# Optimization experiments

Hardware: AMD Instinct MI355X
Metric: run time of the kernel (lower is better)

Reference implementation:

```python
import jax, jax.numpy as jnp
import numpy as np

B = 16384          # tokens
H = 2048           # hidden_size
E = 8              # num_experts
K = 2              # top-k
HF = H // 4        # expert bottleneck dim


def setup_inputs() -> dict:
    key = jax.random.key(0)
    k0, k1, k2, k3 = jax.random.split(key, 4)
    scale = lambda kk, shape, fan: jax.random.normal(kk, shape, jnp.float32) * (1.0 / np.sqrt(fan))
    x = jax.random.normal(k0, (B, H), jnp.float32)
    W1 = scale(k1, (E, H, HF), H)      # experts[e][0].weight (transposed)
    b1 = jnp.zeros((E, HF), jnp.float32)
    W2 = scale(k2, (E, HF), HF)        # experts[e][2].weight (out dim 1, no bias)
    Wg = scale(k3, (H, E), H)          # gate.weight (transposed)
    bg = jnp.zeros((E,), jnp.float32)
    return {"x": x, "W1": W1, "b1": b1, "W2": W2, "Wg": Wg, "bg": bg}


def reference(x, W1, b1, W2, Wg, bg):
    # Gating (eval mode: no noise branch)
    logits = x @ Wg + bg                                  # [B, E]
    top_w, top_i = jax.lax.top_k(logits, K)               # [B, K]
    w = jax.nn.softmax(top_w, axis=-1)                    # [B, K]
    # Scatter top-k softmax weights into dense combine weights [B, E];
    # unselected experts get weight 0, so the dense all-expert compute
    # below is mathematically identical to the masked dispatch loop.
    combine = jnp.zeros_like(logits).at[jnp.arange(x.shape[0])[:, None], top_i].add(w)
    # All-expert MLP: Linear -> exact GELU -> Linear(->1, no bias)
    h = jax.nn.gelu(jnp.einsum('bh,ehf->bef', x, W1) + b1, approximate=False)  # [B, E, HF]
    o = jnp.einsum('bef,ef->be', h, W2)                   # [B, E]
    final_scores = jnp.sum(combine * o, axis=-1, keepdims=True)  # [B, 1]
    return final_scores, logits
```

## Files before the change

kernel.cpp:

```cpp
#include <hip/hip_runtime.h>
#include <math.h>

#define B_TOK 16384
#define H_DIM 2048
#define NE    8
#define TOPK  2
#define HFD   512

#define BK 32
#define NKSTEP (H_DIM / BK)
#define PTMAX 129
#define PROWS 33792

static constexpr size_t OFF_COUNTS = 0;
static constexpr size_t OFF_CBASE  = 128;
static constexpr size_t OFF_BUCKET = 1024;
static constexpr size_t OFF_WSLOT  = 525312;
static constexpr size_t OFF_ROUTE  = 656384;
static constexpr size_t OFF_INV    = 721920;
static constexpr size_t OFF_WGT    = 1u << 20;
static constexpr size_t OFF_P2     = 1572864;
static constexpr size_t OFF_W1H    = 4u << 20;
static constexpr size_t OFF_XGT    = 20971520;

typedef short bfrag __attribute__((ext_vector_type(8)));
typedef float facc  __attribute__((ext_vector_type(16)));

__device__ inline unsigned short f2bf(float f) {
    union { float f; unsigned u; } v; v.f = f;
    unsigned r = v.u + 0x7FFFu + ((v.u >> 16) & 1u);
    return (unsigned short)(r >> 16);
}
__device__ inline unsigned pack2(float lo, float hi) {
    return (unsigned)f2bf(lo) | ((unsigned)f2bf(hi) << 16);
}

__global__ __launch_bounds__(256)
void wg_transpose_kernel(const float* __restrict__ Wg,
                         float* __restrict__ WgT)
{
    const int t = threadIdx.x;
    #pragma unroll
    for (int rep = 0; rep < H_DIM / 256; ++rep) {
        const int h = rep * 256 + t;
        const float4 a = *reinterpret_cast<const float4*>(Wg + (size_t)h * NE);
        const float4 b = *reinterpret_cast<const float4*>(Wg + (size_t)h * NE + 4);
        #pragma unroll
        for (int rr = 0; rr < 8; ++rr) {
            float* W = WgT + (size_t)rr * (NE * H_DIM);
            W[0 * H_DIM + h] = a.x;  W[1 * H_DIM + h] = a.y;
            W[2 * H_DIM + h] = a.z;  W[3 * H_DIM + h] = a.w;
            W[4 * H_DIM + h] = b.x;  W[5 * H_DIM + h] = b.y;
            W[6 * H_DIM + h] = b.z;  W[7 * H_DIM + h] = b.w;
        }
    }
}

__global__ __launch_bounds__(256)
void prep_w1_kernel(const float* __restrict__ W1,
                    unsigned short* __restrict__ W1h)
{
    const int e     = blockIdx.x >> 6;
    const int kstep = blockIdx.x & 63;
    const int tid   = threadIdx.x;

    const float* src = W1 + ((size_t)e * H_DIM + kstep * BK) * HFD;

    #pragma unroll
    for (int s = 0; s < 4; ++s) {
        #pragma unroll
        for (int fh = 0; fh < 2; ++fh) {
            const int f = fh * 256 + tid;
            float v[8];
            #pragma unroll
            for (int j = 0; j < 8; ++j)
                v[j] = src[(size_t)(s * 8 + j) * HFD + f];
            uint4 p;
            p.x = pack2(v[0], v[1]); p.y = pack2(v[2], v[3]);
            p.z = pack2(v[4], v[5]); p.w = pack2(v[6], v[7]);
            *reinterpret_cast<uint4*>(
                W1h + ((size_t)((e * 2 + fh) * 64 + kstep)) * 8192
                    + (s * 256 + tid) * 8) = p;
        }
    }
}

__global__ __launch_bounds__(256)
void gate_logits_kernel(const float* __restrict__ x,
                        const float* __restrict__ WgT,
                        const float* __restrict__ bg,
                        float* __restrict__ out_logits,
                        float* __restrict__ wslot,
                        int*   __restrict__ route)
{
    __shared__ float Wlds[NE * H_DIM];

    const int tid = threadIdx.x;
    const float* Wsrc = WgT + (size_t)(blockIdx.x & 7) * (NE * H_DIM);
    #pragma unroll
    for (int i = 0; i < (NE * H_DIM) / (256 * 4); ++i) {
        const int idx = (i * 256 + tid) * 4;
        *reinterpret_cast<float4*>(&Wlds[idx]) =
            *reinterpret_cast<const float4*>(Wsrc + idx);
    }
    __syncthreads();

    const int w = tid >> 6, l = tid & 63;
    const int tbase = blockIdx.x * 64 + w * 16;

    for (int pass = 0; pass < 4; ++pass) {
        const int t0 = tbase + pass * 4;
        float acc[4][NE];
        #pragma unroll
        for (int j = 0; j < 4; ++j)
            #pragma unroll
            for (int e = 0; e < NE; ++e) acc[j][e] = 0.f;

        for (int i = 0; i < 8; ++i) {
            const int h = i * 256 + 4 * l;
            float4 xv[4];
            #pragma unroll
            for (int j = 0; j < 4; ++j)
                xv[j] = *reinterpret_cast<const float4*>(
                    x + (size_t)(t0 + j) * H_DIM + h);
            #pragma unroll
            for (int e = 0; e < NE; ++e) {
                const float4 wv = *reinterpret_cast<const float4*>(&Wlds[e * H_DIM + h]);
                #pragma unroll
                for (int j = 0; j < 4; ++j)
                    acc[j][e] += xv[j].x * wv.x + xv[j].y * wv.y
                               + xv[j].z * wv.z + xv[j].w * wv.w;
            }
        }

        #pragma unroll
        for (int j = 0; j < 4; ++j)
            #pragma unroll
            for (int e = 0; e < NE; ++e)
                #pragma unroll
                for (int off = 32; off > 0; off >>= 1)
                    acc[j][e] += __shfl_xor(acc[j][e], off, 64);

        if (l == 0) {
            #pragma unroll
            for (int j = 0; j < 4; ++j) {
                const int tok = t0 + j;
                float lg[NE];
                #pragma unroll
                for (int e = 0; e < NE; ++e) lg[e] = acc[j][e] + bg[e];

                float4* lo = reinterpret_cast<float4*>(out_logits + (size_t)tok * NE);
                lo[0] = make_float4(lg[0], lg[1], lg[2], lg[3]);
                lo[1] = make_float4(lg[4], lg[5], lg[6], lg[7]);

                int i0 = 0; float v0 = lg[0];
                #pragma unroll
                for (int e = 1; e < NE; ++e)
                    if (lg[e] > v0) { v0 = lg[e]; i0 = e; }
                int i1 = -1; float v1 = -3.4e38f;
                #pragma unroll
                for (int e = 0; e < NE; ++e)
                    if (e != i0 && lg[e] > v1) { v1 = lg[e]; i1 = e; }

                const float w0 = 1.f / (1.f + expf(v1 - v0));
                wslot[tok * 2]     = w0;
                wslot[tok * 2 + 1] = 1.f - w0;
                route[tok] = i0 | (i1 << 8);
            }
        }
    }
}

__global__ __launch_bounds__(1024)
void route_kernel(const int* __restrict__ route,
                  int* __restrict__ counts,
                  int* __restrict__ bucket)
{
    __shared__ int lcnt[NE];
    __shared__ int lbase[NE];
    const int tid = threadIdx.x;
    const int tok = blockIdx.x * 1024 + tid;

    if (tid < NE) lcnt[tid] = 0;
    __syncthreads();

    const int rt = route[tok];
    const int i0 = rt & 255;
    const int i1 = rt >> 8;
    const int r0 = atomicAdd(&lcnt[i0], 1);
    const int r1 = atomicAdd(&lcnt[i1], 1);
    __syncthreads();

    if (tid < NE) lbase[tid] = atomicAdd(&counts[tid], lcnt[tid]);
    __syncthreads();

    bucket[i0 * B_TOK + lbase[i0] + r0] = tok * 2;
    bucket[i1 * B_TOK + lbase[i1] + r1] = tok * 2 + 1;
}

__global__ void prefix_kernel(const int* __restrict__ counts,
                              int* __restrict__ cbase)
{
    if (threadIdx.x == 0 && blockIdx.x == 0) {
        int acc = 0;
        for (int e = 0; e < NE; ++e) {
            const int cp = ((counts[e] + 127) >> 7) << 7;
            cbase[e]      = acc;
            cbase[NE + e] = cp;
            acc += cp;
        }
    }
}

__global__ __launch_bounds__(256)
void xgather_kernel(const float* __restrict__ x,
                    const int* __restrict__ bucket,
                    const int* __restrict__ counts,
                    const int* __restrict__ cbase,
                    unsigned short* __restrict__ xgT,
                    int* __restrict__ inv)
{
    const int e    = blockIdx.x & 7;
    const int tile = blockIdx.x >> 3;
    const int n    = counts[e];
    const int pos0 = tile * 64;
    if (pos0 >= n) return;
    const int cb   = cbase[e];
    const size_t cpad = (size_t)cbase[NE + e];
    const int t = threadIdx.x;

    __shared__ int toks[64];
    __shared__ unsigned short T[8][64][8];

    if (t < 64) {
        const int pos = pos0 + t;
        const int entry = bucket[e * B_TOK + min(pos, n - 1)];
        toks[t] = entry >> 1;
        if (pos < n) inv[entry] = cb + pos;
    }
    __syncthreads();

    const int p = t >> 2;
    const int q = t & 3;
    const float* src = x + (size_t)toks[p] * H_DIM + q * 16;
    unsigned short* dstbase = xgT + (size_t)cb * H_DIM;

    for (int kc = 0; kc < 32; ++kc) {
        const float4 v0 = *reinterpret_cast<const float4*>(src + kc * 64);
        const float4 v1 = *reinterpret_cast<const float4*>(src + kc * 64 + 4);
        const float4 v2 = *reinterpret_cast<const float4*>(src + kc * 64 + 8);
        const float4 v3 = *reinterpret_cast<const float4*>(src + kc * 64 + 12);
        uint4 pa, pb;
        pa.x = pack2(v0.x, v0.y); pa.y = pack2(v0.z, v0.w);
        pa.z = pack2(v1.x, v1.y); pa.w = pack2(v1.z, v1.w);
        pb.x = pack2(v2.x, v2.y); pb.y = pack2(v2.z, v2.w);
        pb.z = pack2(v3.x, v3.y); pb.w = pack2(v3.z, v3.w);
        __syncthreads();
        *reinterpret_cast<uint4*>(&T[q * 2][p][0])     = pa;
        *reinterpret_cast<uint4*>(&T[q * 2 + 1][p][0]) = pb;
        __syncthreads();
        #pragma unroll
        for (int g = 0; g < 2; ++g) {
            const int u   = t + g * 256;
            const int s8  = u >> 6;
            const int pp  = u & 63;
            const int kst = 2 * kc + (s8 >> 2);
            const int sl  = s8 & 3;
            *reinterpret_cast<uint4*>(
                dstbase + ((size_t)(kst * 4 + sl) * cpad + pos0 + pp) * 8) =
                *reinterpret_cast<const uint4*>(&T[s8][pp][0]);
        }
    }
}

__global__ __launch_bounds__(256, 2)
void expert_mfma_kernel(const unsigned short* __restrict__ xgT,
                        const unsigned short* __restrict__ W1h,
                        const float* __restrict__ b1,
                        const float* __restrict__ W2,
                        const int* __restrict__ counts,
                        const int* __restrict__ cbase,
                        float* __restrict__ P2)
{
    const int e  = blockIdx.x & 7;
    const int r  = blockIdx.x >> 3;
    const int fh = r & 1;
    const int pt = r >> 1;
    const int n  = counts[e];
    const int pos0 = pt * 128;
    if (pos0 >= n) return;
    const int nt = min(128, n - pos0);
    const int cb = cbase[e];
    const size_t cpad = (size_t)cbase[NE + e];

    __shared__ float o_part[2][128];

    const int tid = threadIdx.x;
    const int w   = tid >> 6;
    const int l   = tid & 63;
    const int lo5 = l & 31;
    const int hi  = l >> 5;
    const int wm  = w & 1;
    const int wf  = w >> 1;

    const unsigned short* Wimg = W1h + (size_t)((e * 2 + fh) * 64) * 8192;
    const unsigned short* xg_e = xgT + (size_t)cb * H_DIM;

    const size_t posm0 = (size_t)pos0 + wm * 64 + lo5;
    const size_t posm1 = posm0 + 32;

    facc acc[2][4];
    #pragma unroll
    for (int m = 0; m < 2; ++m)
        #pragma unroll
        for (int fc = 0; fc < 4; ++fc)
            #pragma unroll
            for (int q = 0; q < 16; ++q) acc[m][fc][q] = 0.f;

    #pragma unroll 4
    for (int kk = 0; kk < NKSTEP; ++kk) {
        bfrag xf[2][2];
        #pragma unroll
        for (int c = 0; c < 2; ++c) {
            xf[0][c] = *reinterpret_cast<const bfrag*>(
                xg_e + ((size_t)(kk * 4 + c * 2 + hi) * cpad + posm0) * 8);
            xf[1][c] = *reinterpret_cast<const bfrag*>(
                xg_e + ((size_t)(kk * 4 + c * 2 + hi) * cpad + posm1) * 8);
        }
        bfrag wfr[4][2];
        const unsigned short* wk = Wimg + (size_t)kk * 8192;
        #pragma unroll
        for (int fc = 0; fc < 4; ++fc)
            #pragma unroll
            for (int c = 0; c < 2; ++c)
                wfr[fc][c] = *reinterpret_cast<const bfrag*>(
                    wk + ((c * 2 + hi) * 256 + wf * 128 + fc * 32 + lo5) * 8);

        #pragma unroll
        for (int c = 0; c < 2; ++c)
            #pragma unroll
            for (int m = 0; m < 2; ++m)
                #pragma unroll
                for (int fc = 0; fc < 4; ++fc)
                    acc[m][fc] = __builtin_amdgcn_mfma_f32_32x32x16_bf16(
                        xf[m][c], wfr[fc][c], acc[m][fc], 0, 0, 0);
    }

    const float* b1e = b1 + e * HFD + fh * 256;
    const float* W2e = W2 + e * HFD + fh * 256;
    const float kInvSqrt2 = 0.70710678118654752f;
    float bv[4], wv[4];
    #pragma unroll
    for (int fc = 0; fc < 4; ++fc) {
        const int f = wf * 128 + fc * 32 + lo5;
        bv[fc] = b1e[f];
        wv[fc] = W2e[f];
    }

    #pragma unroll
    for (int m = 0; m < 2; ++m) {
        #pragma unroll
        for (int q = 0; q < 16; ++q) {
            float s = 0.f;
            #pragma unroll
            for (int fc = 0; fc < 4; ++fc) {
                const float h = acc[m][fc][q] + bv[fc];
                s += 0.5f * h * (1.f + erff(h * kInvSqrt2)) * wv[fc];
            }
            #pragma unroll
            for (int off = 16; off > 0; off >>= 1)
                s += __shfl_xor(s, off, 64);
            if (lo5 == 0) {
                const int row = wm * 64 + m * 32 + (q & 3) + 8 * (q >> 2) + 4 * hi;
                o_part[wf][row] = s;
            }
        }
    }
    __syncthreads();

    if (tid < nt)
        P2[(size_t)fh * PROWS + cb + pos0 + tid] =
            o_part[0][tid] + o_part[1][tid];
}

__global__ __launch_bounds__(256)
void combine_kernel(const int* __restrict__ inv,
                    const float* __restrict__ P2,
                    const float* __restrict__ wslot,
                    float* __restrict__ out_scores)
{
    const int t = blockIdx.x * 256 + threadIdx.x;
    if (t >= B_TOK) return;
    const int g0 = inv[2 * t];
    const int g1 = inv[2 * t + 1];
    const float s0 = P2[g0] + P2[PROWS + g0];
    const float s1 = P2[g1] + P2[PROWS + g1];
    out_scores[t] = wslot[2 * t] * s0 + wslot[2 * t + 1] * s1;
}

extern "C" void kernel_launch(void* const* d_in, const int* in_sizes, int n_in,
                              void* d_out, int out_size, void* d_ws, size_t ws_size,
                              hipStream_t stream)
{
    const float* x  = (const float*)d_in[0];
    const float* W1 = (const float*)d_in[1];
    const float* b1 = (const float*)d_in[2];
    const float* W2 = (const float*)d_in[3];
    const float* Wg = (const float*)d_in[4];
    const float* bg = (const float*)d_in[5];

    float* out        = (float*)d_out;
    float* out_scores = out;
    float* out_logits = out + B_TOK;

    char* ws = (char*)d_ws;
    int*            counts = (int*)           (ws + OFF_COUNTS);
    int*            cbase  = (int*)           (ws + OFF_CBASE);
    int*            bucket = (int*)           (ws + OFF_BUCKET);
    float*          wslot  = (float*)         (ws + OFF_WSLOT);
    int*            route  = (int*)           (ws + OFF_ROUTE);
    int*            inv    = (int*)           (ws + OFF_INV);
    float*          WgT    = (float*)         (ws + OFF_WGT);
    float*          P2     = (float*)         (ws + OFF_P2);
    unsigned short* W1h    = (unsigned short*)(ws + OFF_W1H);
    unsigned short* xgT    = (unsigned short*)(ws + OFF_XGT);

    hipMemsetAsync(counts, 0, NE * sizeof(int), stream);

    wg_transpose_kernel<<<1, 256, 0, stream>>>(Wg, WgT);

    prep_w1_kernel<<<NE * NKSTEP, 256, 0, stream>>>(W1, W1h);

    gate_logits_kernel<<<B_TOK / 64, 256, 0, stream>>>(x, WgT, bg, out_logits,
                                                       wslot, route);

    route_kernel<<<B_TOK / 1024, 1024, 0, stream>>>(route, counts, bucket);

    prefix_kernel<<<1, 64, 0, stream>>>(counts, cbase);

    xgather_kernel<<<NE * (B_TOK * 2 / 64), 256, 0, stream>>>(
        x, bucket, counts, cbase, xgT, inv);

    expert_mfma_kernel<<<NE * 2 * PTMAX, 256, 0, stream>>>(
        xgT, W1h, b1, W2, counts, cbase, P2);

    combine_kernel<<<B_TOK / 256, 256, 0, stream>>>(inv, P2, wslot, out_scores);
}
```

Before: 279.9 us.

## Stage expert GEMM tiles through LDS with triple-buffered async global-to-LDS loads

The expert MFMA kernel moves from 256-thread blocks of 128 tokens to 512-thread blocks of 256 tokens. Each K-step's activation and weight tiles are copied into LDS with direct global-to-LDS loads in a three-buffer ring, prefetching two steps ahead and gating with vmcnt waits and barriers. Before, every wave loaded its operands straight from global memory. The aim is to hide memory latency and share each loaded tile across all waves, at the cost of 96KB of LDS per block and one block per CU. Token padding and the partial-output buffer size grow to match the larger tile.

```diff
diff --git a/kernel.cpp b/kernel.cpp
--- a/kernel.cpp
+++ b/kernel.cpp
@@ -9,8 +9,8 @@
 
 #define BK 32
 #define NKSTEP (H_DIM / BK)
-#define PTMAX 129
-#define PROWS 33792
+#define PTMAX 65
+#define PROWS 35840
 
 static constexpr size_t OFF_COUNTS = 0;
 static constexpr size_t OFF_CBASE  = 128;
@@ -35,6 +35,12 @@
     return (unsigned)f2bf(lo) | ((unsigned)f2bf(hi) << 16);
 }
 
+__device__ __forceinline__ void gload_lds16(const void* g, void* l) {
+    __builtin_amdgcn_global_load_lds(
+        (const __attribute__((address_space(1))) unsigned int*)g,
+        (__attribute__((address_space(3))) unsigned int*)l, 16, 0, 0);
+}
+
 __global__ __launch_bounds__(256)
 void wg_transpose_kernel(const float* __restrict__ Wg,
                          float* __restrict__ WgT)
@@ -69,8 +75,8 @@
     #pragma unroll
     for (int s = 0; s < 4; ++s) {
         #pragma unroll
-        for (int fh = 0; fh < 2; ++fh) {
-            const int f = fh * 256 + tid;
+        for (int fn = 0; fn < 2; ++fn) {
+            const int f = fn * 256 + tid;
             float v[8];
             #pragma unroll
             for (int j = 0; j < 8; ++j)
@@ -79,7 +85,7 @@
             p.x = pack2(v[0], v[1]); p.y = pack2(v[2], v[3]);
             p.z = pack2(v[4], v[5]); p.w = pack2(v[6], v[7]);
             *reinterpret_cast<uint4*>(
-                W1h + ((size_t)((e * 2 + fh) * 64 + kstep)) * 8192
+                W1h + ((size_t)((e * 2 + fn) * 64 + kstep)) * 8192
                     + (s * 256 + tid) * 8) = p;
         }
     }
@@ -204,7 +210,7 @@
     if (threadIdx.x == 0 && blockIdx.x == 0) {
         int acc = 0;
         for (int e = 0; e < NE; ++e) {
-            const int cp = ((counts[e] + 127) >> 7) << 7;
+            const int cp = ((counts[e] + 255) >> 8) << 8;
             cbase[e]      = acc;
             cbase[NE + e] = cp;
             acc += cp;
@@ -273,7 +279,7 @@
     }
 }
 
-__global__ __launch_bounds__(256, 2)
+__global__ __launch_bounds__(512, 1)
 void expert_mfma_kernel(const unsigned short* __restrict__ xgT,
                         const unsigned short* __restrict__ W1h,
                         const float* __restrict__ b1,
@@ -284,16 +290,18 @@
 {
     const int e  = blockIdx.x & 7;
     const int r  = blockIdx.x >> 3;
-    const int fh = r & 1;
+    const int fn = r & 1;
     const int pt = r >> 1;
     const int n  = counts[e];
-    const int pos0 = pt * 128;
+    const int pos0 = pt * 256;
     if (pos0 >= n) return;
-    const int nt = min(128, n - pos0);
+    const int nt = min(256, n - pos0);
     const int cb = cbase[e];
     const size_t cpad = (size_t)cbase[NE + e];
 
-    __shared__ float o_part[2][128];
+    __shared__ unsigned short Xb[3][8192];
+    __shared__ unsigned short Wb[3][8192];
+    __shared__ float o_part[4][256];
 
     const int tid = threadIdx.x;
     const int w   = tid >> 6;
@@ -301,86 +309,115 @@
     const int lo5 = l & 31;
     const int hi  = l >> 5;
     const int wm  = w & 1;
-    const int wf  = w >> 1;
-
-    const unsigned short* Wimg = W1h + (size_t)((e * 2 + fh) * 64) * 8192;
+    const int wn  = w >> 1;
+
+    const unsigned short* Wimg = W1h + (size_t)((e * 2 + fn) * 64) * 8192;
     const unsigned short* xg_e = xgT + (size_t)cb * H_DIM;
 
-    const size_t posm0 = (size_t)pos0 + wm * 64 + lo5;
-    const size_t posm1 = posm0 + 32;
-
-    facc acc[2][4];
-    #pragma unroll
-    for (int m = 0; m < 2; ++m)
-        #pragma unroll
-        for (int fc = 0; fc < 4; ++fc)
-            #pragma unroll
-            for (int q = 0; q < 16; ++q) acc[m][fc][q] = 0.f;
-
-    #pragma unroll 4
+    const int u0 = tid, u1 = 512 + tid;
+    const int xs0 = u0 >> 8, xp0 = u0 & 255;
+    const int xs1 = u1 >> 8, xp1 = u1 & 255;
+
+    facc acc[4][2];
+    #pragma unroll
+    for (int m = 0; m < 4; ++m)
+        #pragma unroll
+        for (int nn = 0; nn < 2; ++nn)
+            #pragma unroll
+            for (int q = 0; q < 16; ++q) acc[m][nn][q] = 0.f;
+
+    #define STAGE(KK, B) do {                                                  \
+        gload_lds16(xg_e + ((size_t)((KK) * 4 + xs0) * cpad + pos0 + xp0) * 8, \
+                    &Xb[B][u0 * 8]);                                           \
+        gload_lds16(xg_e + ((size_t)((KK) * 4 + xs1) * cpad + pos0 + xp1) * 8, \
+                    &Xb[B][u1 * 8]);                                           \
+        gload_lds16(Wimg + (size_t)(KK) * 8192 + u0 * 8, &Wb[B][u0 * 8]);      \
+        gload_lds16(Wimg + (size_t)(KK) * 8192 + u1 * 8, &Wb[B][u1 * 8]);      \
+    } while (0)
+
+    #define COMPUTE(B) do {                                                    \
+        _Pragma("unroll")                                                      \
+        for (int ks = 0; ks < 2; ++ks) {                                       \
+            const int slot = ks * 2 + hi;                                      \
+            bfrag a[4], wf[2];                                                 \
+            _Pragma("unroll")                                                  \
+            for (int m = 0; m < 4; ++m)                                        \
+                a[m] = *reinterpret_cast<const bfrag*>(                        \
+                    &Xb[B][(slot * 256 + wm * 128 + m * 32 + lo5) * 8]);       \
+            _Pragma("unroll")                                                  \
+            for (int nn = 0; nn < 2; ++nn)                                     \
+                wf[nn] = *reinterpret_cast<const bfrag*>(                      \
+                    &Wb[B][(slot * 256 + wn * 64 + nn * 32 + lo5) * 8]);       \
+            _Pragma("unroll")                                                  \
+            for (int m = 0; m < 4; ++m)                                        \
+                _Pragma("unroll")                                              \
+                for (int nn = 0; nn < 2; ++nn)                                 \
+                    acc[m][nn] = __builtin_amdgcn_mfma_f32_32x32x16_bf16(      \
+                        a[m], wf[nn], acc[m][nn], 0, 0, 0);                    \
+        }                                                                      \
+    } while (0)
+
+    STAGE(0, 0);
+    STAGE(1, 1);
+    asm volatile("s_waitcnt vmcnt(4)" ::: "memory");
+    __builtin_amdgcn_s_barrier();
+
+    int cur = 0;
     for (int kk = 0; kk < NKSTEP; ++kk) {
-        bfrag xf[2][2];
-        #pragma unroll
-        for (int c = 0; c < 2; ++c) {
-            xf[0][c] = *reinterpret_cast<const bfrag*>(
-                xg_e + ((size_t)(kk * 4 + c * 2 + hi) * cpad + posm0) * 8);
-            xf[1][c] = *reinterpret_cast<const bfrag*>(
-                xg_e + ((size_t)(kk * 4 + c * 2 + hi) * cpad + posm1) * 8);
-        }
-        bfrag wfr[4][2];
-        const unsigned short* wk = Wimg + (size_t)kk * 8192;
-        #pragma unroll
-        for (int fc = 0; fc < 4; ++fc)
-            #pragma unroll
-            for (int c = 0; c < 2; ++c)
-                wfr[fc][c] = *reinterpret_cast<const bfrag*>(
-                    wk + ((c * 2 + hi) * 256 + wf * 128 + fc * 32 + lo5) * 8);
-
-        #pragma unroll
-        for (int c = 0; c < 2; ++c)
-            #pragma unroll
-            for (int m = 0; m < 2; ++m)
-                #pragma unroll
-                for (int fc = 0; fc < 4; ++fc)
-                    acc[m][fc] = __builtin_amdgcn_mfma_f32_32x32x16_bf16(
-                        xf[m][c], wfr[fc][c], acc[m][fc], 0, 0, 0);
-    }
-
-    const float* b1e = b1 + e * HFD + fh * 256;
-    const float* W2e = W2 + e * HFD + fh * 256;
+        const int nxt = (cur + 2 >= 3) ? cur - 1 : cur + 2;
+        if (kk + 2 < NKSTEP) STAGE(kk + 2, nxt);
+
+        __builtin_amdgcn_s_setprio(1);
+        COMPUTE(cur);
+        __builtin_amdgcn_s_setprio(0);
+
+        if (kk + 1 < NKSTEP) {
+            if (kk + 2 < NKSTEP)
+                asm volatile("s_waitcnt vmcnt(4)" ::: "memory");
+            else
+                asm volatile("s_waitcnt vmcnt(0)" ::: "memory");
+            __builtin_amdgcn_s_barrier();
+        }
+        cur = (cur + 1 >= 3) ? 0 : cur + 1;
+    }
+    #undef STAGE
+    #undef COMPUTE
+
+    const float* b1e = b1 + e * HFD + fn * 256;
+    const float* W2e = W2 + e * HFD + fn * 256;
     const float kInvSqrt2 = 0.70710678118654752f;
-    float bv[4], wv[4];
-    #pragma unroll
-    for (int fc = 0; fc < 4; ++fc) {
-        const int f = wf * 128 + fc * 32 + lo5;
-        bv[fc] = b1e[f];
-        wv[fc] = W2e[f];
-    }
-
-    #pragma unroll
-    for (int m = 0; m < 2; ++m) {
+    float bv[2], wv[2];
+    #pragma unroll
+    for (int nn = 0; nn < 2; ++nn) {
+        const int f = wn * 64 + nn * 32 + lo5;
+        bv[nn] = b1e[f];
+        wv[nn] = W2e[f];
+    }
+
+    #pragma unroll
+    for (int m = 0; m < 4; ++m) {
         #pragma unroll
         for (int q = 0; q < 16; ++q) {
             float s = 0.f;
             #pragma unroll
-            for (int fc = 0; fc < 4; ++fc) {
-                const float h = acc[m][fc][q] + bv[fc];
-                s += 0.5f * h * (1.f + erff(h * kInvSqrt2)) * wv[fc];
+            for (int nn = 0; nn < 2; ++nn) {
+                const float h = acc[m][nn][q] + bv[nn];
+                s += 0.5f * h * (1.f + erff(h * kInvSqrt2)) * wv[nn];
             }
             #pragma unroll
             for (int off = 16; off > 0; off >>= 1)
                 s += __shfl_xor(s, off, 64);
             if (lo5 == 0) {
-                const int row = wm * 64 + m * 32 + (q & 3) + 8 * (q >> 2) + 4 * hi;
-                o_part[wf][row] = s;
+                const int row = wm * 128 + m * 32 + (q & 3) + 8 * (q >> 2) + 4 * hi;
+                o_part[wn][row] = s;
             }
         }
     }
     __syncthreads();
 
     if (tid < nt)
-        P2[(size_t)fh * PROWS + cb + pos0 + tid] =
-            o_part[0][tid] + o_part[1][tid];
+        P2[(size_t)fn * PROWS + cb + pos0 + tid] =
+            ((o_part[0][tid] + o_part[1][tid]) + o_part[2][tid]) + o_part[3][tid];
 }
 
 __global__ __launch_bounds__(256)
@@ -441,7 +478,7 @@
     xgather_kernel<<<NE * (B_TOK * 2 / 64), 256, 0, stream>>>(
         x, bucket, counts, cbase, xgT, inv);
 
-    expert_mfma_kernel<<<NE * 2 * PTMAX, 256, 0, stream>>>(
+    expert_mfma_kernel<<<NE * 2 * PTMAX, 512, 0, stream>>>(
         xgT, W1h, b1, W2, counts, cbase, P2);
 
     combine_kernel<<<B_TOK / 256, 256, 0, stream>>>(inv, P2, wslot, out_scores);
```

Result: slower. 370.0 us (+32.2%).
